# Kernel tuning notes

Measured on AMD Instinct MI355X. Metric: run time of the kernel, lower is better.

The kernel has to match this reference:

```python
import jax, jax.numpy as jnp
import numpy as np

# SDNet-CTRL cfg constants
MU = 0.1          # FISTA step size (cfg['MODEL']['MU'])
LMBD = 0.1        # sparsity weight (cfg['MODEL']['LAMBDA'][0])
N_STEPS = 4       # FISTA iterations (cfg['MODEL']['NUM_LAYERS'])
EPS_BN = 1e-5


def _conv(x, w, stride, padding):
    # torch F.conv2d, NCHW / OIHW
    return jax.lax.conv_general_dilated(
        x, w, window_strides=(stride, stride),
        padding=[(padding, padding), (padding, padding)],
        dimension_numbers=('NCHW', 'OIHW', 'NCHW'))


def _conv_t(c, w, stride, padding):
    # torch F.conv_transpose2d(c, w, stride, padding) with output_padding chosen
    # so that it exactly inverts the spatial map of _conv (k=4,s=2,p=1 -> 0).
    k = w.shape[2]
    w_t = jnp.flip(w, (2, 3)).transpose(1, 0, 2, 3)  # (I,O,k,k) flipped
    pad = k - 1 - padding
    return jax.lax.conv_general_dilated(
        c, w_t, window_strides=(1, 1),
        padding=[(pad, pad), (pad, pad)],
        lhs_dilation=(stride, stride),
        dimension_numbers=('NCHW', 'OIHW', 'NCHW'))


def _shrink_nn(c, thr):
    # non-negative soft threshold (cfg NONEGATIVE=True)
    return jax.nn.relu(c - thr)


def _dict_conv(x, w, stride, padding):
    # DictBlock: FISTA convolutional sparse coding, n_dict=1, w_norm=True.
    # normalize each dictionary atom (output filter) to unit l2 norm
    wn = w * jax.lax.rsqrt(jnp.sum(w * w, axis=(1, 2, 3), keepdims=True))
    ss = MU
    thr = LMBD * ss
    # t = 0
    c = _shrink_nn(ss * _conv(x, wn, stride, padding), thr)
    c_pre_pre = jnp.zeros_like(c)
    c_pre = c
    tk = 1.0
    for t in range(1, N_STEPS):
        tk_pre = tk
        tk = (1.0 + float(np.sqrt(1.0 + 4.0 * tk_pre * tk_pre))) / 2.0
        y = c_pre + ((tk_pre - 1.0) / tk) * (c_pre - c_pre_pre)
        r = x - _conv_t(y, wn, stride, padding)      # residual in image space
        c = _shrink_nn(y + ss * _conv(r, wn, stride, padding), thr)
        c_pre_pre, c_pre = c_pre, c
    return c


def _bn(x, g, b):
    # training-mode BatchNorm2d (batch statistics)
    m = jnp.mean(x, axis=(0, 2, 3), keepdims=True)
    v = jnp.var(x, axis=(0, 2, 3), keepdims=True)
    return g.reshape(1, -1, 1, 1) * (x - m) * jax.lax.rsqrt(v + EPS_BN) + b.reshape(1, -1, 1, 1)


def _lrelu(x):
    return jnp.where(x >= 0, x, 0.2 * x)


def setup_inputs() -> dict:
    key = jax.random.key(0)
    ks = jax.random.split(key, 5)
    nc, ndf, nz = 3, 128, 256
    B, H = 256, 32

    def mk_w(k, o, i):
        return jax.random.normal(k, (o, i, 4, 4), jnp.float32) * 0.02

    return {
        'x': jax.random.normal(ks[0], (B, nc, H, H), jnp.float32),
        'w1': mk_w(ks[1], ndf, nc),
        'w2': mk_w(ks[2], 2 * ndf, ndf),
        'w3': mk_w(ks[3], 4 * ndf, 2 * ndf),
        'w4': mk_w(ks[4], nz, 4 * ndf),
        'g2': jnp.ones((2 * ndf,), jnp.float32),
        'b2': jnp.zeros((2 * ndf,), jnp.float32),
        'g3': jnp.ones((4 * ndf,), jnp.float32),
        'b3': jnp.zeros((4 * ndf,), jnp.float32),
    }


def reference(x, w1, w2, w3, w4, g2, b2, g3, b3):
    h = _lrelu(_dict_conv(x, w1, 2, 1))                 # (B, ndf, 16, 16)
    h = _lrelu(_bn(_dict_conv(h, w2, 2, 1), g2, b2))    # (B, 2ndf, 8, 8)
    h = _lrelu(_bn(_dict_conv(h, w3, 2, 1), g3, b3))    # (B, 4ndf, 4, 4)
    h = _dict_conv(h, w4, 1, 0)                         # (B, nz, 1, 1)
    h = h.reshape(h.shape[0], -1)                       # Flatten
    n = jnp.sqrt(jnp.sum(h * h, axis=1, keepdims=True))
    return h / jnp.maximum(n, 1e-12)                    # F.normalize(dim=1)
```

## Files before the change

### kernel.cpp

```cpp
#include <hip/hip_runtime.h>
#include <math.h>

#define SS   0.1f
#define THRC 0.01f

typedef __attribute__((ext_vector_type(8))) short s16x8;
typedef __attribute__((ext_vector_type(4))) float f32x4;

__device__ __forceinline__ float b2f(unsigned short u){
  union{unsigned int i; float f;} v; v.i = ((unsigned int)u)<<16; return v.f;
}
__device__ __forceinline__ unsigned short f2b(float f){
  union{float f; unsigned int i;} v; v.f = f;
  return (unsigned short)((v.i + 0x7fffu + ((v.i>>16)&1u))>>16);
}
__device__ __forceinline__ s16x8 as_s16x8(uint4 u){
  union{uint4 a; s16x8 b;} c; c.a = u; return c.b;
}
__device__ __forceinline__ int swz8(int row, int q){ return (row<<3) | (q ^ (row&7)); }

__device__ __forceinline__ void gld16(const void* g, void* l){
  __builtin_amdgcn_global_load_lds(
      (const __attribute__((address_space(1))) unsigned int*)g,
      (__attribute__((address_space(3))) unsigned int*)l, 16, 0, 0);
}

enum { EPI_FIRST=0, EPI_UPDATE=1, EPI_PARTIAL=2, EPI_TPART=3, EPI_RES_FLAT=4 };

struct EpiM {
  unsigned short* C;
  const unsigned short* Y;
  const unsigned short* Cprev;
  unsigned short* Yout;
  const unsigned short* img;
  const unsigned short* zp;
  float coef;
  int S_MN, Kc, lgS;
};

struct LA_ident {
  const unsigned short* A; int K;
  __device__ void setz(int){}
  __device__ __forceinline__ const unsigned short* addr(int m, int k8) const {
    return A + (size_t)m*K + ((size_t)k8<<3);
  }
};
struct LA_nhwc {
  const unsigned short* img; const unsigned short* zp; int lH, lW, lC;
  __device__ void setz(int){}
  __device__ __forceinline__ const unsigned short* addr(int m, int k8) const {
    int lWo = lW-1, lHo = lH-1;
    int wo = m & ((1<<lWo)-1); int t = m>>lWo; int ho = t & ((1<<lHo)-1); int b = t>>lHo;
    int k = k8<<3; int kk = k>>lC; int i = k & ((1<<lC)-1);
    int kw = kk&3, kh = kk>>2;
    int h = 2*ho + kh - 1, w = 2*wo + kw - 1;
    if ((unsigned)h >= (1u<<lH) || (unsigned)w >= (1u<<lW)) return zp;
    return img + (((((((size_t)b<<lH)|h)<<lW)|w))<<lC) + i;
  }
};
struct LA_yg {
  const unsigned short* y; const unsigned short* zp; int lHo, lWo, lO, ph, pw;
  __device__ void setz(int z){ ph = z>>1; pw = z&1; }
  __device__ __forceinline__ const unsigned short* addr(int m, int k8) const {
    int l = m & ((1<<lWo)-1); int t = m>>lWo; int j = t & ((1<<lHo)-1); int b = t>>lHo;
    int k = k8<<3; int tt = k>>lO; int o = k & ((1<<lO)-1);
    int th = tt>>1, tw = tt&1;
    int ho = ph ? (j+1-th) : (j-th);
    int wo = pw ? (l+1-tw) : (l-tw);
    if ((unsigned)ho >= (1u<<lHo) || (unsigned)wo >= (1u<<lWo)) return zp;
    return y + (((((((size_t)b<<lHo)|ho)<<lWo)|wo))<<lO) + o;
  }
};
struct LA_padb {
  const unsigned short* img;
  __device__ void setz(int){}
  __device__ __forceinline__ const unsigned short* addr(int m, int k8) const {
    int wo = m&15, t = m>>4, ho = t&15, b = t>>4;
    int kh = k8>>1, kw0 = (k8&1)<<1;
    int h = 2*ho + kh, w = 2*wo + kw0;
    return img + (((size_t)b*34 + h)*34 + w)*4;
  }
};

template<class AL, int EPI>
__global__ __launch_bounds__(512)
void mgemm_k(AL al, const unsigned short* __restrict__ Bw, int M, int N, int K, EpiM ep)
{
  __shared__ uint4 As[1024];
  __shared__ uint4 Bs[1024];
  const int tid = threadIdx.x;
  const int bm = blockIdx.y<<7, bn = blockIdx.x<<7;
  const int z = blockIdx.z;
  int kb = 0, ke = K;
  const unsigned short* Bp = Bw;
  if (EPI == EPI_PARTIAL){ kb = z*ep.Kc; ke = kb + ep.Kc; }
  if (EPI == EPI_TPART){
    int cls = z >> ep.lgS, kz = z & ((1<<ep.lgS)-1);
    Bp = Bw + (size_t)cls*(size_t)N*K; al.setz(cls);
    kb = kz*ep.Kc; ke = kb + ep.Kc;
  }

  f32x4 acc[4][2];
  #pragma unroll
  for (int i=0;i<4;++i)
    #pragma unroll
    for (int j=0;j<2;++j){ acc[i][j][0]=0.f; acc[i][j][1]=0.f; acc[i][j][2]=0.f; acc[i][j][3]=0.f; }

  const int lane = tid & 63, wid = tid >> 6;
  const int wm = (wid>>2)<<6, wn = (wid&3)<<5;
  const int fr = lane & 15, fq = lane >> 4;

  auto issueA = [&](int k0){
    int k8 = k0>>3;
    #pragma unroll
    for (int i=0;i<2;++i){
      int s  = (wid<<7) + (i<<6) + lane;
      int sr = s>>3, q = (s&7) ^ (sr&7);
      gld16(al.addr(bm+sr, k8+q), (void*)&As[(wid<<7) + (i<<6)]);
    }
  };
  auto issueB = [&](int k0){
    int k8 = k0>>3;
    #pragma unroll
    for (int i=0;i<2;++i){
      int s  = (wid<<7) + (i<<6) + lane;
      int sr = s>>3, q = (s&7) ^ (sr&7);
      int gn = bn + sr;
      const unsigned short* src = (gn < N) ? Bp + (size_t)gn*K + ((size_t)(k8+q)<<3) : ep.zp;
      gld16(src, (void*)&Bs[(wid<<7) + (i<<6)]);
    }
  };

  for (int k0 = kb; k0 < ke; k0 += 64){
    issueA(k0); issueB(k0);
    asm volatile("s_waitcnt vmcnt(0)" ::: "memory");
    __builtin_amdgcn_s_barrier();
    __builtin_amdgcn_sched_barrier(0);
    #pragma unroll
    for (int half=0; half<2; ++half){
      const int qb = (half<<2) | fq;
      s16x8 af[4], bf[2];
      #pragma unroll
      for (int mi=0;mi<4;++mi) af[mi] = as_s16x8(As[swz8(wm + mi*16 + fr, qb)]);
      #pragma unroll
      for (int ni=0;ni<2;++ni) bf[ni] = as_s16x8(Bs[swz8(wn + ni*16 + fr, qb)]);
      #pragma unroll
      for (int mi=0;mi<4;++mi)
        #pragma unroll
        for (int ni=0;ni<2;++ni)
          acc[mi][ni] = __builtin_amdgcn_mfma_f32_16x16x32_bf16(af[mi], bf[ni], acc[mi][ni], 0,0,0);
    }
    if (k0 + 64 < ke){
      __builtin_amdgcn_s_barrier();
      __builtin_amdgcn_sched_barrier(0);
    }
  }

  #pragma unroll
  for (int mi=0;mi<4;++mi){
    #pragma unroll
    for (int ni=0;ni<2;++ni){
      int n = bn + wn + ni*16 + fr;
      if (n >= N) continue;
      int mb = bm + wm + mi*16 + (fq<<2);
      #pragma unroll
      for (int r=0;r<4;++r){
        int m = mb + r;
        float a = acc[mi][ni][r];
        if (EPI == EPI_FIRST){
          float v = SS*a - THRC; v = v>0.f ? v : 0.f;
          ep.C[(size_t)m*N + n] = f2b(v);
        } else if (EPI == EPI_UPDATE){
          size_t idx = (size_t)m*N + n;
          float v = b2f(ep.Y[idx]) + SS*a - THRC; v = v>0.f ? v : 0.f;
          ep.C[idx] = f2b(v);
          if (ep.Yout) ep.Yout[idx] = f2b(v + ep.coef*(v - b2f(ep.Cprev[idx])));
        } else if (EPI == EPI_PARTIAL || EPI == EPI_TPART){
          ep.C[(size_t)z*ep.S_MN + (size_t)m*N + n] = f2b(a);
        } else {
          size_t ridx = (size_t)m*N + n;
          ep.C[ridx] = f2b(b2f(ep.img[ridx]) - a);
        }
      }
    }
  }
}

__global__ __launch_bounds__(64)
void wnorm1_k(const float* __restrict__ w, unsigned short* __restrict__ wf1,
              unsigned short* __restrict__ wcolT)
{
  int o = blockIdx.x, tid = threadIdx.x;
  __shared__ float red[64];
  float v = (tid < 48) ? w[(size_t)o*48 + tid] : 0.f;
  red[tid] = v*v; __syncthreads();
  for (int d=32; d>0; d>>=1){ if (tid<d) red[tid] += red[tid+d]; __syncthreads(); }
  float nv = v * rsqrtf(red[0]);
  if (tid < 48){
    int c = tid>>4, t = tid&15;
    wf1[(size_t)o*64 + t*4 + c] = f2b(nv);
    wcolT[(size_t)(t*4+c)*128 + o] = f2b(nv);
  } else {
    int t = tid - 48;
    wf1[(size_t)o*64 + t*4 + 3] = 0;
    wcolT[(size_t)(t*4+3)*128 + o] = 0;
  }
}
__global__ __launch_bounds__(256)
void wnormX_k(const float* __restrict__ w, int Cin, int O,
              unsigned short* __restrict__ wT, unsigned short* __restrict__ wclsT,
              unsigned short* __restrict__ wEO)
{
  int o = blockIdx.x, tid = threadIdx.x; int E = Cin*16;
  __shared__ float red[256];
  float s = 0.f;
  for (int e = tid; e < E; e += 256){ float v = w[(size_t)o*E + e]; s += v*v; }
  red[tid] = s; __syncthreads();
  for (int d=128; d>0; d>>=1){ if (tid<d) red[tid] += red[tid+d]; __syncthreads(); }
  float scale = rsqrtf(red[0]);
  for (int e = tid; e < E; e += 256){
    float v = w[(size_t)o*E + e] * scale;
    int i = e>>4, t = e&15, kh = t>>2, kw = t&3;
    int ee = t*Cin + i;
    if (wT)  wT[(size_t)o*E + ee] = f2b(v);
    if (wEO) wEO[(size_t)ee*O + o] = f2b(v);
    if (wclsT){
      int ph = (kh&1)^1, pw = (kw&1)^1, cls = ph*2+pw;
      int tt = (kh>>1)*2 + (kw>>1);
      wclsT[(((size_t)cls*Cin + i)*4 + tt)*O + o] = f2b(v);
    }
  }
}

__global__ void splitk_shrink_k(const unsigned short* __restrict__ part,
                                const unsigned short* __restrict__ Y,
                                unsigned short* __restrict__ C,
                                unsigned short* __restrict__ Yout,
                                const unsigned short* __restrict__ Cprev,
                                float coef, int MN, int S)
{
  int total8 = MN>>3;
  for (int i8 = blockIdx.x*blockDim.x + threadIdx.x; i8 < total8; i8 += gridDim.x*blockDim.x){
    size_t off = (size_t)i8<<3;
    float s[8];
    #pragma unroll
    for (int j=0;j<8;++j) s[j]=0.f;
    for (int zz = 0; zz < S; ++zz){
      uint4 pv = *(const uint4*)(part + (size_t)zz*MN + off);
      const unsigned short* pe = (const unsigned short*)&pv;
      #pragma unroll
      for (int j=0;j<8;++j) s[j] += b2f(pe[j]);
    }
    uint4 yv = make_uint4(0,0,0,0), cp = make_uint4(0,0,0,0);
    if (Y)    yv = *(const uint4*)(Y + off);
    if (Yout) cp = *(const uint4*)(Cprev + off);
    const unsigned short* ye = (const unsigned short*)&yv;
    const unsigned short* ce = (const unsigned short*)&cp;
    unsigned short co[8], yo[8];
    #pragma unroll
    for (int j=0;j<8;++j){
      float v = (Y ? b2f(ye[j]) : 0.f) + SS*s[j] - THRC; v = v>0.f ? v : 0.f;
      co[j] = f2b(v);
      if (Yout) yo[j] = f2b(v + coef*(v - b2f(ce[j])));
    }
    *(uint4*)(C + off) = *(const uint4*)co;
    if (Yout) *(uint4*)(Yout + off) = *(const uint4*)yo;
  }
}

__global__ void tcomb_k(const unsigned short* __restrict__ part,
                        const unsigned short* __restrict__ img,
                        unsigned short* __restrict__ outp,
                        int lH, int lW, int lC, int S, int MN, int total8)
{
  for (int i8 = blockIdx.x*blockDim.x + threadIdx.x; i8 < total8; i8 += gridDim.x*blockDim.x){
    size_t idx = (size_t)i8<<3;
    int c = (int)(idx & ((1u<<lC)-1));
    int w = (int)(idx>>lC) & ((1<<lW)-1);
    int h = (int)(idx>>(lC+lW)) & ((1<<lH)-1);
    int b = (int)(idx>>(lC+lW+lH));
    int j = h>>1, l = w>>1, cls = ((h&1)<<1)|(w&1);
    int m = (((b<<(lH-1))|j)<<(lW-1))|l;
    int N = 1<<lC;
    const unsigned short* pb = part + ((size_t)cls*S)*MN + (size_t)m*N + c;
    float s[8];
    #pragma unroll
    for (int q=0;q<8;++q) s[q]=0.f;
    for (int kz=0; kz<S; ++kz){
      uint4 pv = *(const uint4*)(pb + (size_t)kz*MN);
      const unsigned short* pe = (const unsigned short*)&pv;
      #pragma unroll
      for (int q=0;q<8;++q) s[q] += b2f(pe[q]);
    }
    uint4 iv = *(const uint4*)(img + idx);
    const unsigned short* ie = (const unsigned short*)&iv;
    unsigned short ro[8];
    #pragma unroll
    for (int q=0;q<8;++q) ro[q] = f2b(b2f(ie[q]) - s[q]);
    *(uint4*)(outp + idx) = *(const uint4*)ro;
  }
}

__global__ void pad_x_k(const float* __restrict__ x, unsigned short* __restrict__ xpb){
  int idx = blockIdx.x*256 + threadIdx.x;
  if (idx >= 262144) return;
  int w = idx&31, t = idx>>5, h = t&31, b = t>>5;
  size_t src = (size_t)b*3072 + h*32 + w;
  unsigned short* d = xpb + (((size_t)b*34 + h+1)*34 + w+1)*4;
  d[0] = f2b(x[src]); d[1] = f2b(x[src+1024]); d[2] = f2b(x[src+2048]); d[3] = 0;
}

__global__ void l1_resid_k(const unsigned short* __restrict__ Col,
                           const float* __restrict__ x, unsigned short* __restrict__ r1pb)
{
  int idx = blockIdx.x*256 + threadIdx.x;
  if (idx >= 262144) return;
  int w = idx&31, t = idx>>5, h = t&31, b = t>>5;
  float a0=0.f, a1=0.f, a2=0.f;
  #pragma unroll
  for (int kh=0; kh<4; ++kh){
    int hh = h+1-kh; if (hh & 1) continue; int ho = hh>>1; if ((unsigned)ho >= 16u) continue;
    #pragma unroll
    for (int kw=0; kw<4; ++kw){
      int ww = w+1-kw; if (ww & 1) continue; int wo = ww>>1; if ((unsigned)wo >= 16u) continue;
      int m = (b*16+ho)*16+wo;
      const unsigned short* cp = Col + (size_t)m*64 + (kh*4+kw)*4;
      a0 += b2f(cp[0]); a1 += b2f(cp[1]); a2 += b2f(cp[2]);
    }
  }
  size_t src = (size_t)b*3072 + h*32 + w;
  unsigned short* d = r1pb + (((size_t)b*34 + h+1)*34 + w+1)*4;
  d[0] = f2b(x[src] - a0); d[1] = f2b(x[src+1024] - a1); d[2] = f2b(x[src+2048] - a2); d[3] = 0;
}

__global__ void bn_stats_k(const unsigned short* __restrict__ d, float* __restrict__ sums,
                           int rows, int O){
  for (int c = threadIdx.x; c < O; c += blockDim.x){
    float a = 0.f, b = 0.f;
    for (int r = blockIdx.x; r < rows; r += gridDim.x){
      float v = b2f(d[(size_t)r*O + c]); a += v; b += v*v;
    }
    atomicAdd(&sums[c], a); atomicAdd(&sums[O+c], b);
  }
}
__global__ void bn_apply_k(const unsigned short* __restrict__ d, const float* __restrict__ sums,
                           const float* __restrict__ g, const float* __restrict__ bta,
                           unsigned short* __restrict__ outp, int rows, int O, float inv_cnt){
  int total = rows*O;
  for (int i = blockIdx.x*blockDim.x + threadIdx.x; i < total; i += gridDim.x*blockDim.x){
    int c = i % O;
    float mean = sums[c]*inv_cnt;
    float var  = sums[O+c]*inv_cnt - mean*mean;
    float v = g[c]*(b2f(d[i])-mean)*rsqrtf(var + 1e-5f) + bta[c];
    outp[i] = f2b(v >= 0.f ? v : 0.2f*v);
  }
}

__global__ __launch_bounds__(256)
void norm_rows_k(const unsigned short* __restrict__ h, float* __restrict__ out){
  int row = blockIdx.x, tid = threadIdx.x;
  __shared__ float red[256];
  float v = b2f(h[(size_t)row*256 + tid]);
  red[tid] = v*v; __syncthreads();
  for (int d=128; d>0; d>>=1){ if (tid<d) red[tid] += red[tid+d]; __syncthreads(); }
  float nrm = sqrtf(red[0]); nrm = nrm > 1e-12f ? nrm : 1e-12f;
  out[(size_t)row*256 + tid] = v / nrm;
}

extern "C" void kernel_launch(void* const* d_in, const int* in_sizes, int n_in,
                              void* d_out, int out_size, void* d_ws, size_t ws_size,
                              hipStream_t stream)
{
  const float* x  = (const float*)d_in[0];
  const float* w1 = (const float*)d_in[1];
  const float* w2 = (const float*)d_in[2];
  const float* w3 = (const float*)d_in[3];
  const float* w4 = (const float*)d_in[4];
  const float* g2 = (const float*)d_in[5];
  const float* b2 = (const float*)d_in[6];
  const float* g3 = (const float*)d_in[7];
  const float* b3 = (const float*)d_in[8];
  float* out = (float*)d_out;

  char* p = (char*)d_ws;
  auto ah = [&](size_t n){ unsigned short* r = (unsigned short*)p; p += n*2; return r; };
  auto af = [&](size_t n){ float* r = (float*)p; p += n*4; return r; };

  unsigned short* wf1    = ah(128*64);
  unsigned short* wcol1T = ah(64*128);
  unsigned short* wT2    = ah((size_t)256*2048);
  unsigned short* wcls2  = ah((size_t)4*128*1024);
  unsigned short* wT3    = ah((size_t)512*4096);
  unsigned short* wcls3  = ah((size_t)4*256*2048);
  unsigned short* wT4    = ah((size_t)256*8192);
  unsigned short* wE4    = ah((size_t)8192*256);
  unsigned short* h1     = ah((size_t)8388608);
  unsigned short* h2     = ah((size_t)4194304);
  unsigned short* h3     = ah((size_t)2097152);
  unsigned short* cA     = ah((size_t)8388608);
  unsigned short* cB     = ah((size_t)8388608);
  unsigned short* yA     = ah((size_t)8388608);
  unsigned short* yB     = ah((size_t)8388608);
  unsigned short* rH     = ah((size_t)8388608);
  char* regionA = p; p += 33554432;
  unsigned short* Col    = (unsigned short*)regionA;
  unsigned short* xpb    = (unsigned short*)(regionA + 8388608);
  unsigned short* r1pb   = (unsigned short*)(regionA + 8388608 + 2367488);
  unsigned short* partB  = (unsigned short*)regionA;
  float* bnsum = af(1024);
  unsigned short* zp16 = ah(128);

  double tk = 1.0; float coef[4] = {0.f,0.f,0.f,0.f};
  for (int t = 1; t < 4; ++t){
    double tkp = tk; tk = (1.0 + sqrt(1.0 + 4.0*tkp*tkp))*0.5;
    coef[t] = (float)((tkp - 1.0)/tk);
  }

  hipMemsetAsync(zp16, 0, 256, stream);
  hipMemsetAsync(xpb,  0, 2367488, stream);
  hipMemsetAsync(r1pb, 0, 2367488, stream);
  pad_x_k<<<1024,256,0,stream>>>(x, xpb);
  wnorm1_k<<<128, 64, 0, stream>>>(w1, wf1, wcol1T);
  wnormX_k<<<256,256,0,stream>>>(w2, 128, 256, wT2, wcls2, nullptr);
  wnormX_k<<<512,256,0,stream>>>(w3, 256, 512, wT3, wcls3, nullptr);
  wnormX_k<<<256,256,0,stream>>>(w4, 512, 256, wT4, nullptr, wE4);

  auto l1_fwd = [&](const unsigned short* src, const unsigned short* Y, const unsigned short* Cp,
                    unsigned short* Cout, unsigned short* Yout, float cf){
    LA_padb al{src};
    EpiM ep{}; ep.C=Cout; ep.Y=Y; ep.Cprev=Cp; ep.Yout=Yout; ep.coef=cf; ep.zp=zp16;
    dim3 g(1, 512, 1);
    if (Y) mgemm_k<LA_padb,EPI_UPDATE><<<g,512,0,stream>>>(al, wf1, 65536,128,64, ep);
    else   mgemm_k<LA_padb,EPI_FIRST ><<<g,512,0,stream>>>(al, wf1, 65536,128,64, ep);
  };
  auto l1_tconv = [&](const unsigned short* y){
    LA_ident al{y, 128};
    EpiM ep{}; ep.C=Col; ep.S_MN=0; ep.Kc=128; ep.zp=zp16;
    mgemm_k<LA_ident,EPI_PARTIAL><<<dim3(1,512,1),512,0,stream>>>(al, wcol1T, 65536,64,128, ep);
    l1_resid_k<<<1024,256,0,stream>>>(Col, x, r1pb);
  };
  l1_fwd(xpb,  nullptr, nullptr, cA, nullptr, 0.f);
  l1_tconv(cA);
  l1_fwd(r1pb, cA, cA, cB, yA, coef[2]);
  l1_tconv(yA);
  l1_fwd(r1pb, yA, cB, cA, yB, coef[3]);
  l1_tconv(yB);
  l1_fwd(r1pb, yB, nullptr, h1, nullptr, 0.f);

  auto l2_fwd = [&](const unsigned short* src, const unsigned short* Y, const unsigned short* Cp,
                    unsigned short* Cout, unsigned short* Yout, float cf){
    LA_nhwc al{src, zp16, 4,4,7};
    EpiM ep{}; ep.C=partB; ep.S_MN=16384*256; ep.Kc=512; ep.zp=zp16;
    mgemm_k<LA_nhwc,EPI_PARTIAL><<<dim3(2,128,4),512,0,stream>>>(al, wT2, 16384,256,2048, ep);
    splitk_shrink_k<<<2048,256,0,stream>>>(partB, Y, Cout, Yout, Cp, cf, 16384*256, 4);
  };
  auto l2_tconv = [&](const unsigned short* y){
    LA_yg al{y, zp16, 3,3,8, 0,0};
    EpiM ep{}; ep.C=partB; ep.S_MN=16384*128; ep.Kc=512; ep.lgS=1; ep.zp=zp16;
    mgemm_k<LA_yg,EPI_TPART><<<dim3(1,128,8),512,0,stream>>>(al, wcls2, 16384,128,1024, ep);
    tcomb_k<<<2048,256,0,stream>>>(partB, h1, rH, 4,4,7, 2, 16384*128, 1048576);
  };
  l2_fwd(h1, nullptr, nullptr, cA, nullptr, 0.f);
  l2_tconv(cA);
  l2_fwd(rH, cA, cA, cB, yA, coef[2]);
  l2_tconv(yA);
  l2_fwd(rH, yA, cB, cA, yB, coef[3]);
  l2_tconv(yB);
  l2_fwd(rH, yB, nullptr, cB, nullptr, 0.f);
  hipMemsetAsync(bnsum, 0, 2*256*sizeof(float), stream);
  bn_stats_k<<<256,256,0,stream>>>(cB, bnsum, 16384, 256);
  bn_apply_k<<<2048,256,0,stream>>>(cB, bnsum, g2, b2, h2, 16384, 256, 1.f/16384.f);

  auto l3_fwd = [&](const unsigned short* src, const unsigned short* Y, const unsigned short* Cp,
                    unsigned short* Cout, unsigned short* Yout, float cf){
    LA_nhwc al{src, zp16, 3,3,8};
    EpiM ep{}; ep.C=partB; ep.S_MN=4096*512; ep.Kc=512; ep.zp=zp16;
    mgemm_k<LA_nhwc,EPI_PARTIAL><<<dim3(4,32,8),512,0,stream>>>(al, wT3, 4096,512,4096, ep);
    splitk_shrink_k<<<1024,256,0,stream>>>(partB, Y, Cout, Yout, Cp, cf, 4096*512, 8);
  };
  auto l3_tconv = [&](const unsigned short* y){
    LA_yg al{y, zp16, 2,2,9, 0,0};
    EpiM ep{}; ep.C=partB; ep.S_MN=4096*256; ep.Kc=512; ep.lgS=2; ep.zp=zp16;
    mgemm_k<LA_yg,EPI_TPART><<<dim3(2,32,16),512,0,stream>>>(al, wcls3, 4096,256,2048, ep);
    tcomb_k<<<2048,256,0,stream>>>(partB, h2, rH, 3,3,8, 4, 4096*256, 524288);
  };
  l3_fwd(h2, nullptr, nullptr, cA, nullptr, 0.f);
  l3_tconv(cA);
  l3_fwd(rH, cA, cA, cB, yA, coef[2]);
  l3_tconv(yA);
  l3_fwd(rH, yA, cB, cA, yB, coef[3]);
  l3_tconv(yB);
  l3_fwd(rH, yB, nullptr, cB, nullptr, 0.f);
  hipMemsetAsync(bnsum, 0, 2*512*sizeof(float), stream);
  bn_stats_k<<<256,256,0,stream>>>(cB, bnsum, 4096, 512);
  bn_apply_k<<<2048,256,0,stream>>>(cB, bnsum, g3, b3, h3, 4096, 512, 1.f/4096.f);

  auto l4_fwd = [&](const unsigned short* Asrc, const unsigned short* Y, const unsigned short* Cp,
                    unsigned short* Cout, unsigned short* Yout, float cf){
    LA_ident al{Asrc, 8192};
    EpiM ep{}; ep.C=partB; ep.S_MN=65536; ep.Kc=128; ep.zp=zp16;
    mgemm_k<LA_ident,EPI_PARTIAL><<<dim3(2,2,64),512,0,stream>>>(al, wT4, 256,256,8192, ep);
    splitk_shrink_k<<<32,256,0,stream>>>(partB, Y, Cout, Yout, Cp, cf, 65536, 64);
  };
  auto l4_tconv = [&](const unsigned short* y){
    LA_ident al{y, 256};
    EpiM ep{}; ep.C=rH; ep.img=h3; ep.zp=zp16;
    mgemm_k<LA_ident,EPI_RES_FLAT><<<dim3(64,2,1),512,0,stream>>>(al, wE4, 256,8192,256, ep);
  };
  l4_fwd(h3, nullptr, nullptr, cA, nullptr, 0.f);
  l4_tconv(cA);
  l4_fwd(rH, cA, cA, cB, yA, coef[2]);
  l4_tconv(yA);
  l4_fwd(rH, yA, cB, cA, yB, coef[3]);
  l4_tconv(yB);
  l4_fwd(rH, yB, nullptr, cB, nullptr, 0.f);

  norm_rows_k<<<256,256,0,stream>>>(cB, out);
}
```

Measured before the change: 912.4 us.

## Replace layer-4 FISTA conv/transpose-conv pairs with precomputed Gram matrix updates

Layer 4 is a 1x1-output conv, so the FISTA update y + ss*W(x - W^T y) is rewritten as y + ss*Wx - ss*(W W^T) y. The code computes b = ss*W x and the 256x256 Gram matrix G = W W^T once, each as a split-K GEMM followed by a combine kernel. Each remaining iteration then becomes one small 256x256x256 GEMM with a fused shrink/momentum epilogue. This replaces three large K=8192 split-K GEMMs and three transpose-conv GEMMs. The trade-off is extra bf16 rounding in G and b, which can shift numerics.

```diff
diff --git a/kernel.cpp b/kernel.cpp
--- a/kernel.cpp
+++ b/kernel.cpp
@@ -25,7 +25,7 @@
       (__attribute__((address_space(3))) unsigned int*)l, 16, 0, 0);
 }
 
-enum { EPI_FIRST=0, EPI_UPDATE=1, EPI_PARTIAL=2, EPI_TPART=3, EPI_RES_FLAT=4 };
+enum { EPI_FIRST=0, EPI_UPDATE=1, EPI_PARTIAL=2, EPI_TPART=3, EPI_GRAM=4 };
 
 struct EpiM {
   unsigned short* C;
@@ -178,8 +178,10 @@
         } else if (EPI == EPI_PARTIAL || EPI == EPI_TPART){
           ep.C[(size_t)z*ep.S_MN + (size_t)m*N + n] = f2b(a);
         } else {
-          size_t ridx = (size_t)m*N + n;
-          ep.C[ridx] = f2b(b2f(ep.img[ridx]) - a);
+          size_t idx = (size_t)m*N + n;
+          float v = b2f(ep.Y[idx]) + b2f(ep.img[idx]) - SS*a - THRC; v = v>0.f ? v : 0.f;
+          ep.C[idx] = f2b(v);
+          if (ep.Yout) ep.Yout[idx] = f2b(v + ep.coef*(v - b2f(ep.Cprev[idx])));
         }
       }
     }
@@ -268,6 +270,39 @@
   }
 }
 
+__global__ void combine_k(const unsigned short* __restrict__ part,
+                          unsigned short* __restrict__ out1,
+                          unsigned short* __restrict__ out2,
+                          int MN, int S, int mode)
+{
+  int total8 = MN>>3;
+  for (int i8 = blockIdx.x*blockDim.x + threadIdx.x; i8 < total8; i8 += gridDim.x*blockDim.x){
+    size_t off = (size_t)i8<<3;
+    float s[8];
+    #pragma unroll
+    for (int j=0;j<8;++j) s[j]=0.f;
+    for (int zz = 0; zz < S; ++zz){
+      uint4 pv = *(const uint4*)(part + (size_t)zz*MN + off);
+      const unsigned short* pe = (const unsigned short*)&pv;
+      #pragma unroll
+      for (int j=0;j<8;++j) s[j] += b2f(pe[j]);
+    }
+    unsigned short o1[8], o2[8];
+    #pragma unroll
+    for (int j=0;j<8;++j){
+      if (mode == 0){ o1[j] = f2b(s[j]); }
+      else {
+        float bsc = SS*s[j];
+        o1[j] = f2b(bsc);
+        float v = bsc - THRC; v = v>0.f ? v : 0.f;
+        o2[j] = f2b(v);
+      }
+    }
+    *(uint4*)(out1 + off) = *(const uint4*)o1;
+    if (mode == 1) *(uint4*)(out2 + off) = *(const uint4*)o2;
+  }
+}
+
 __global__ void tcomb_k(const unsigned short* __restrict__ part,
                         const unsigned short* __restrict__ img,
                         unsigned short* __restrict__ outp,
@@ -393,7 +428,8 @@
   unsigned short* wT3    = ah((size_t)512*4096);
   unsigned short* wcls3  = ah((size_t)4*256*2048);
   unsigned short* wT4    = ah((size_t)256*8192);
-  unsigned short* wE4    = ah((size_t)8192*256);
+  unsigned short* Gm     = ah((size_t)256*256);
+  unsigned short* bb     = ah((size_t)65536);
   unsigned short* h1     = ah((size_t)8388608);
   unsigned short* h2     = ah((size_t)4194304);
   unsigned short* h3     = ah((size_t)2097152);
@@ -423,7 +459,7 @@
   wnorm1_k<<<128, 64, 0, stream>>>(w1, wf1, wcol1T);
   wnormX_k<<<256,256,0,stream>>>(w2, 128, 256, wT2, wcls2, nullptr);
   wnormX_k<<<512,256,0,stream>>>(w3, 256, 512, wT3, wcls3, nullptr);
-  wnormX_k<<<256,256,0,stream>>>(w4, 512, 256, wT4, nullptr, wE4);
+  wnormX_k<<<256,256,0,stream>>>(w4, 512, 256, wT4, nullptr, nullptr);
 
   auto l1_fwd = [&](const unsigned short* src, const unsigned short* Y, const unsigned short* Cp,
                     unsigned short* Cout, unsigned short* Yout, float cf){
@@ -495,25 +531,28 @@
   bn_stats_k<<<256,256,0,stream>>>(cB, bnsum, 4096, 512);
   bn_apply_k<<<2048,256,0,stream>>>(cB, bnsum, g3, b3, h3, 4096, 512, 1.f/4096.f);
 
-  auto l4_fwd = [&](const unsigned short* Asrc, const unsigned short* Y, const unsigned short* Cp,
-                    unsigned short* Cout, unsigned short* Yout, float cf){
-    LA_ident al{Asrc, 8192};
-    EpiM ep{}; ep.C=partB; ep.S_MN=65536; ep.Kc=128; ep.zp=zp16;
-    mgemm_k<LA_ident,EPI_PARTIAL><<<dim3(2,2,64),512,0,stream>>>(al, wT4, 256,256,8192, ep);
-    splitk_shrink_k<<<32,256,0,stream>>>(partB, Y, Cout, Yout, Cp, cf, 65536, 64);
-  };
-  auto l4_tconv = [&](const unsigned short* y){
-    LA_ident al{y, 256};
-    EpiM ep{}; ep.C=rH; ep.img=h3; ep.zp=zp16;
-    mgemm_k<LA_ident,EPI_RES_FLAT><<<dim3(64,2,1),512,0,stream>>>(al, wE4, 256,8192,256, ep);
-  };
-  l4_fwd(h3, nullptr, nullptr, cA, nullptr, 0.f);
-  l4_tconv(cA);
-  l4_fwd(rH, cA, cA, cB, yA, coef[2]);
-  l4_tconv(yA);
-  l4_fwd(rH, yA, cB, cA, yB, coef[3]);
-  l4_tconv(yB);
-  l4_fwd(rH, yB, nullptr, cB, nullptr, 0.f);
+  {
+    LA_ident al{h3, 8192};
+    EpiM ep{}; ep.C=partB; ep.S_MN=65536; ep.Kc=256; ep.zp=zp16;
+    mgemm_k<LA_ident,EPI_PARTIAL><<<dim3(2,2,32),512,0,stream>>>(al, wT4, 256,256,8192, ep);
+    combine_k<<<32,256,0,stream>>>(partB, bb, cA, 65536, 32, 1);
+  }
+  {
+    LA_ident al{wT4, 8192};
+    EpiM ep{}; ep.C=partB; ep.S_MN=65536; ep.Kc=256; ep.zp=zp16;
+    mgemm_k<LA_ident,EPI_PARTIAL><<<dim3(2,2,32),512,0,stream>>>(al, wT4, 256,256,8192, ep);
+    combine_k<<<32,256,0,stream>>>(partB, Gm, nullptr, 65536, 32, 0);
+  }
+  auto l4_gram = [&](const unsigned short* Y, const unsigned short* Cp,
+                     unsigned short* Cout, unsigned short* Yout, float cf){
+    LA_ident al{Y, 256};
+    EpiM ep{}; ep.C=Cout; ep.Y=Y; ep.Cprev=Cp; ep.Yout=Yout; ep.coef=cf;
+    ep.img=bb; ep.zp=zp16;
+    mgemm_k<LA_ident,EPI_GRAM><<<dim3(2,2,1),512,0,stream>>>(al, Gm, 256,256,256, ep);
+  };
+  l4_gram(cA, cA, cB, yA, coef[2]);
+  l4_gram(yA, cB, cA, yB, coef[3]);
+  l4_gram(yB, nullptr, cB, nullptr, 0.f);
 
   norm_rows_k<<<256,256,0,stream>>>(cB, out);
 }
```

New measurement: 826.0 us. 1.1x faster.
